# Kernel optimization log

Hardware: AMD Instinct MI355X
Metric: run time of the kernel (lower is better)

The kernel has to match this reference:

```python
import jax, jax.numpy as jnp
import numpy as np

STRIDE = 2  # ksize = [1, STRIDE, 1, 1]: unpool along height only
B, H, W, C = 8, 512, 256, 64


def setup_inputs() -> dict:
    key = jax.random.key(0)
    k1, k2 = jax.random.split(key)
    inputs = jax.random.normal(k1, (B, H, W, C), dtype=jnp.float32)
    # TF argmax-style flat indices into the per-batch output grid [2H, W, C]
    mask = jax.random.randint(k2, (B, H, W, C), 0, STRIDE * H * W * C, dtype=jnp.int64)
    return {"inputs": inputs, "mask": mask}


def reference(inputs, mask):
    b_, h, w, c = inputs.shape
    out_h = h * STRIDE  # output_shape = (B, stride*H, W, C)
    # Decode flat per-batch indices exactly as the TF layer does
    y = mask // (w * c)
    x = (mask % (w * c)) // c
    b = jnp.arange(b_, dtype=jnp.int64)[:, None, None, None]  # batch_range
    f = jnp.arange(c, dtype=jnp.int64)                        # feature_range
    # tf.scatter_nd sums duplicate indices; .at[].add matches that semantics
    out = jnp.zeros((b_, out_h, w, c), dtype=inputs.dtype)
    out = out.at[b, y, x, f].add(inputs)
    return out
```

## Files before the change

### kernel.cpp

```cpp
#include <hip/hip_runtime.h>


typedef unsigned int u32;
typedef unsigned short u16;
typedef unsigned long long u64;

typedef int   iv4 __attribute__((ext_vector_type(4)));
typedef float fv4 __attribute__((ext_vector_type(4)));

constexpr long long N_IN = 1LL << 26;
constexpr int SBS   = 8192;
constexpr int NSB   = (int)(N_IN / SBS);
constexpr int NBKT  = 1024;
constexpr int NWIN  = 8192;
constexpr int RSH   = 14;
constexpr int RSLOTS = 1 << RSH;
constexpr int SB_PER_B = 1024;

constexpr size_t OFF_RECA = 0;
constexpr size_t OFF_DIR  = (size_t)N_IN * 8;
constexpr size_t OFF_DIRT = OFF_DIR + (size_t)NSB * NBKT * 2;
constexpr size_t WS_FUSED = OFF_DIRT + (size_t)NWIN * SB_PER_B * 2;

__global__ __launch_bounds__(512) void passA(const float* __restrict__ in,
                                             const int* __restrict__ mask,
                                             u64* __restrict__ recA,
                                             u16* __restrict__ dir)
{
    __shared__ u32 cur[NBKT];
    __shared__ u32 wsum[8];
    __shared__ u64 sRec[SBS];
    const int tid = threadIdx.x;
    const int sb  = blockIdx.x;
    const int e0  = sb * SBS + tid * 16;

    const iv4* m4 = (const iv4*)mask + (e0 >> 2);
    const fv4* v4 = (const fv4*)in + (e0 >> 2);
    iv4 m0 = __builtin_nontemporal_load(m4 + 0);
    iv4 m1 = __builtin_nontemporal_load(m4 + 1);
    iv4 m2 = __builtin_nontemporal_load(m4 + 2);
    iv4 m3 = __builtin_nontemporal_load(m4 + 3);
    fv4 va = __builtin_nontemporal_load(v4 + 0);
    fv4 vb = __builtin_nontemporal_load(v4 + 1);
    fv4 vc = __builtin_nontemporal_load(v4 + 2);
    fv4 vd = __builtin_nontemporal_load(v4 + 3);
    const u32 bbits = ((u32)(e0 >> 23)) << 24;
    const u32 c0 = (u32)(e0 & 63);

    u32 tg[16]; float vv[16];
    tg[ 0] = bbits + (((u32)m0.x) & ~63u) + c0 +  0; vv[ 0] = va.x;
    tg[ 1] = bbits + (((u32)m0.y) & ~63u) + c0 +  1; vv[ 1] = va.y;
    tg[ 2] = bbits + (((u32)m0.z) & ~63u) + c0 +  2; vv[ 2] = va.z;
    tg[ 3] = bbits + (((u32)m0.w) & ~63u) + c0 +  3; vv[ 3] = va.w;
    tg[ 4] = bbits + (((u32)m1.x) & ~63u) + c0 +  4; vv[ 4] = vb.x;
    tg[ 5] = bbits + (((u32)m1.y) & ~63u) + c0 +  5; vv[ 5] = vb.y;
    tg[ 6] = bbits + (((u32)m1.z) & ~63u) + c0 +  6; vv[ 6] = vb.z;
    tg[ 7] = bbits + (((u32)m1.w) & ~63u) + c0 +  7; vv[ 7] = vb.w;
    tg[ 8] = bbits + (((u32)m2.x) & ~63u) + c0 +  8; vv[ 8] = vc.x;
    tg[ 9] = bbits + (((u32)m2.y) & ~63u) + c0 +  9; vv[ 9] = vc.y;
    tg[10] = bbits + (((u32)m2.z) & ~63u) + c0 + 10; vv[10] = vc.z;
    tg[11] = bbits + (((u32)m2.w) & ~63u) + c0 + 11; vv[11] = vc.w;
    tg[12] = bbits + (((u32)m3.x) & ~63u) + c0 + 12; vv[12] = vd.x;
    tg[13] = bbits + (((u32)m3.y) & ~63u) + c0 + 13; vv[13] = vd.y;
    tg[14] = bbits + (((u32)m3.z) & ~63u) + c0 + 14; vv[14] = vd.z;
    tg[15] = bbits + (((u32)m3.w) & ~63u) + c0 + 15; vv[15] = vd.w;

    cur[2 * tid] = 0;
    cur[2 * tid + 1] = 0;
    __syncthreads();
#pragma unroll
    for (int j = 0; j < 16; ++j) atomicAdd(&cur[(tg[j] >> RSH) & (NBKT - 1)], 1u);
    __syncthreads();

    {
        const int lane = tid & 63;
        const int wid  = tid >> 6;
        u32 a = cur[2 * tid];
        u32 b = cur[2 * tid + 1];
        u32 sum = a + b;
        u32 s = sum;
#pragma unroll
        for (int d = 1; d < 64; d <<= 1) {
            u32 n = __shfl_up(s, (unsigned)d, 64);
            if (lane >= d) s += n;
        }
        if (lane == 63) wsum[wid] = s;
        u32 exw = s - sum;
        __syncthreads();
        if (tid == 0) {
            u32 run = 0;
#pragma unroll
            for (int w = 0; w < 8; ++w) { u32 t2 = wsum[w]; wsum[w] = run; run += t2; }
        }
        __syncthreads();
        u32 start = wsum[wid] + exw;
        dir[(size_t)sb * NBKT + 2 * tid]     = (u16)start;
        dir[(size_t)sb * NBKT + 2 * tid + 1] = (u16)(start + a);
        cur[2 * tid]     = start;
        cur[2 * tid + 1] = start + a;
    }
    __syncthreads();

#pragma unroll
    for (int j = 0; j < 16; ++j) {
        u32 p = atomicAdd(&cur[(tg[j] >> RSH) & (NBKT - 1)], 1u);
        sRec[p] = ((u64)(tg[j] & (RSLOTS - 1)) << 32) | (u64)__float_as_uint(vv[j]);
    }
    __syncthreads();
#pragma unroll
    for (int k = 0; k < 16; ++k) {
        int i = tid + k * 512;
        recA[(size_t)sb * SBS + i] = sRec[i];
    }
}

__global__ __launch_bounds__(256) void tposeD(const u16* __restrict__ dir,
                                              u16* __restrict__ dirT)
{
    __shared__ u16 t[64][65];
    const int tx = threadIdx.x;
    const int ty = threadIdx.y;
    const int bb = blockIdx.z;
    const int sb0 = blockIdx.x * 64;
    const int lb0 = blockIdx.y * 64;
#pragma unroll
    for (int k = 0; k < 16; ++k) {
        int row = k * 4 + ty;
        t[row][tx] = dir[((size_t)(bb * SB_PER_B + sb0 + row)) * NBKT + lb0 + tx];
    }
    __syncthreads();
#pragma unroll
    for (int k = 0; k < 16; ++k) {
        int row = k * 4 + ty;
        dirT[((size_t)(bb * NBKT + lb0 + row)) * SB_PER_B + sb0 + tx] = t[tx][row];
    }
}

__global__ __launch_bounds__(1024, 8) void passC(const u64* __restrict__ recA,
                                                 const u16* __restrict__ dirT,
                                                 float* __restrict__ out)
{
    __shared__ float acc[RSLOTS];
    __shared__ u32 cSrc[SB_PER_B];
    __shared__ u16 cLen[SB_PER_B];
    const int tid = threadIdx.x;
    const int bid = blockIdx.x;
    const int w   = ((bid & 7) << 10) | (bid >> 3);
    const int bb  = w >> 10;
    const int lb  = w & (NBKT - 1);

    {
        u32 st = dirT[(size_t)w * SB_PER_B + tid];
        u32 en = (lb == NBKT - 1) ? (u32)SBS : (u32)dirT[(size_t)(w + 1) * SB_PER_B + tid];
        cSrc[tid] = (u32)(bb * SB_PER_B + tid) * (u32)SBS + st;
        cLen[tid] = (u16)(en - st);
    }
    {
        fv4 z = {0.f, 0.f, 0.f, 0.f};
        fv4* av = (fv4*)acc;
#pragma unroll
        for (int i = tid; i < RSLOTS / 4; i += 1024) av[i] = z;
    }
    __syncthreads();

    const int g  = tid >> 4;
    const int gl = tid & 15;
#pragma unroll
    for (int r = 0; r < 2; ++r) {
        u32 src[8]; int len[8]; u64 rec[8];
#pragma unroll
        for (int j = 0; j < 8; ++j) {
            int s = g + (r * 8 + j) * 64;
            src[j] = cSrc[s];
            len[j] = (int)cLen[s];
        }
#pragma unroll
        for (int j = 0; j < 8; ++j) rec[j] = recA[src[j] + gl];
#pragma unroll
        for (int j = 0; j < 8; ++j) {
            if (gl < len[j])
                atomicAdd(&acc[(u32)(rec[j] >> 32)], __uint_as_float((u32)rec[j]));
        }
#pragma unroll
        for (int j = 0; j < 8; ++j) {
            for (int off = gl + 16; off < len[j]; off += 16) {
                u64 rc = recA[src[j] + off];
                atomicAdd(&acc[(u32)(rc >> 32)], __uint_as_float((u32)rc));
            }
        }
    }
    __syncthreads();

    fv4* o4 = (fv4*)out + ((size_t)w << (RSH - 2));
    const fv4* a4 = (const fv4*)acc;
#pragma unroll
    for (int i = tid; i < RSLOTS / 4; i += 1024)
        __builtin_nontemporal_store(a4[i], o4 + i);
}

__global__ __launch_bounds__(256) void unmaxpool_scatter(
    const float* __restrict__ in, const int* __restrict__ mask,
    float* __restrict__ out)
{
    const long long n4 = N_IN / 4;
    long long gidx = (long long)blockIdx.x * blockDim.x + threadIdx.x;
    const long long stride = (long long)gridDim.x * blockDim.x;
    for (; gidx < n4; gidx += stride) {
        float4 v = reinterpret_cast<const float4*>(in)[gidx];
        int4 m = reinterpret_cast<const int4*>(mask)[gidx];
        long long i0 = gidx * 4;
        u32 ob = ((u32)(i0 >> 23)) << 24;
        u32 c0 = (u32)(i0 & 63);
        atomicAdd(&out[ob + (u32)(m.x & ~63) + c0 + 0], v.x);
        atomicAdd(&out[ob + (u32)(m.y & ~63) + c0 + 1], v.y);
        atomicAdd(&out[ob + (u32)(m.z & ~63) + c0 + 2], v.z);
        atomicAdd(&out[ob + (u32)(m.w & ~63) + c0 + 3], v.w);
    }
}

extern "C" void kernel_launch(void* const* d_in, const int* in_sizes, int n_in,
                              void* d_out, int out_size, void* d_ws, size_t ws_size,
                              hipStream_t stream) {
    const float* in = (const float*)d_in[0];
    const int* mask = (const int*)d_in[1];
    float* out = (float*)d_out;
    char* ws = (char*)d_ws;

    if (d_ws != nullptr && ws_size >= WS_FUSED) {
        u64* recA = (u64*)(ws + OFF_RECA);
        u16* dir  = (u16*)(ws + OFF_DIR);
        u16* dirT = (u16*)(ws + OFF_DIRT);
        passA<<<NSB, 512, 0, stream>>>(in, mask, recA, dir);
        tposeD<<<dim3(16, 16, 8), dim3(64, 4), 0, stream>>>(dir, dirT);
        passC<<<NWIN, 1024, 0, stream>>>(recA, dirT, out);
    } else {
        (void)hipMemsetAsync(out, 0, (size_t)out_size * sizeof(float), stream);
        unmaxpool_scatter<<<2048, 256, 0, stream>>>(in, mask, out);
    }
}
```

Before: 632.5 us.

## Load-balance passC record gathering via prefix-sum over segment lengths

Replaces the fixed 16-lanes-per-segment gather in passC with an exclusive prefix sum over per-superblock segment lengths. Each thread writes the source indices for its segment into a shared index buffer in 1024-entry rounds, and the whole block then processes one record per thread. This is meant to remove lane divergence and idle lanes from uneven segment lengths (about 8 records on average). In exchange it adds a block-wide scan, a serial per-thread fill loop, and two barriers per round, which may cost more than the imbalance it removes.

```diff
diff --git a/kernel.cpp b/kernel.cpp
--- a/kernel.cpp
+++ b/kernel.cpp
@@ -141,20 +141,31 @@
                                                  float* __restrict__ out)
 {
     __shared__ float acc[RSLOTS];
-    __shared__ u32 cSrc[SB_PER_B];
-    __shared__ u16 cLen[SB_PER_B];
+    __shared__ u32 cPre[SB_PER_B + 1];
+    __shared__ u32 srcIdx[1024];
+    __shared__ u32 wsum[16];
     const int tid = threadIdx.x;
     const int bid = blockIdx.x;
     const int w   = ((bid & 7) << 10) | (bid >> 3);
     const int bb  = w >> 10;
     const int lb  = w & (NBKT - 1);
 
-    {
-        u32 st = dirT[(size_t)w * SB_PER_B + tid];
-        u32 en = (lb == NBKT - 1) ? (u32)SBS : (u32)dirT[(size_t)(w + 1) * SB_PER_B + tid];
-        cSrc[tid] = (u32)(bb * SB_PER_B + tid) * (u32)SBS + st;
-        cLen[tid] = (u16)(en - st);
-    }
+    const u32 st = dirT[(size_t)w * SB_PER_B + tid];
+    const u32 en = (lb == NBKT - 1) ? (u32)SBS : (u32)dirT[(size_t)(w + 1) * SB_PER_B + tid];
+    const u32 len = en - st;
+    const u32 src = (u32)(bb * SB_PER_B + tid) * (u32)SBS + st;
+
+    const int lane = tid & 63;
+    const int wid  = tid >> 6;
+    u32 s = len;
+#pragma unroll
+    for (int d = 1; d < 64; d <<= 1) {
+        u32 n = __shfl_up(s, (unsigned)d, 64);
+        if (lane >= d) s += n;
+    }
+    if (lane == 63) wsum[wid] = s;
+    const u32 exw = s - len;
+
     {
         fv4 z = {0.f, 0.f, 0.f, 0.f};
         fv4* av = (fv4*)acc;
@@ -162,34 +173,34 @@
         for (int i = tid; i < RSLOTS / 4; i += 1024) av[i] = z;
     }
     __syncthreads();
-
-    const int g  = tid >> 4;
-    const int gl = tid & 15;
-#pragma unroll
-    for (int r = 0; r < 2; ++r) {
-        u32 src[8]; int len[8]; u64 rec[8];
-#pragma unroll
-        for (int j = 0; j < 8; ++j) {
-            int s = g + (r * 8 + j) * 64;
-            src[j] = cSrc[s];
-            len[j] = (int)cLen[s];
+    if (tid == 0) {
+        u32 run = 0;
+#pragma unroll
+        for (int ww = 0; ww < 16; ++ww) { u32 t2 = wsum[ww]; wsum[ww] = run; run += t2; }
+    }
+    __syncthreads();
+    const u32 pre = wsum[wid] + exw;
+    cPre[tid] = pre;
+    if (tid == SB_PER_B - 1) cPre[SB_PER_B] = pre + len;
+    __syncthreads();
+    const u32 total = cPre[SB_PER_B];
+    const int nsub = (int)((total + 1023u) >> 10);
+
+    for (int r = 0; r < nsub; ++r) {
+        const u32 r0 = (u32)r << 10;
+        const u32 r1 = r0 + 1024u;
+        u32 lo = pre > r0 ? pre : r0;
+        u32 hi = (pre + len < r1) ? (pre + len) : r1;
+        for (u32 q = lo; q < hi; ++q) srcIdx[q - r0] = src + (q - pre);
+        __syncthreads();
+        u32 n = total - r0; if (n > 1024u) n = 1024u;
+        if ((u32)tid < n) {
+            u32 si = srcIdx[tid];
+            u64 rec = recA[si];
+            atomicAdd(&acc[(u32)(rec >> 32)], __uint_as_float((u32)rec));
         }
-#pragma unroll
-        for (int j = 0; j < 8; ++j) rec[j] = recA[src[j] + gl];
-#pragma unroll
-        for (int j = 0; j < 8; ++j) {
-            if (gl < len[j])
-                atomicAdd(&acc[(u32)(rec[j] >> 32)], __uint_as_float((u32)rec[j]));
-        }
-#pragma unroll
-        for (int j = 0; j < 8; ++j) {
-            for (int off = gl + 16; off < len[j]; off += 16) {
-                u64 rc = recA[src[j] + off];
-                atomicAdd(&acc[(u32)(rc >> 32)], __uint_as_float((u32)rc));
-            }
-        }
-    }
-    __syncthreads();
+        __syncthreads();
+    }
 
     fv4* o4 = (fv4*)out + ((size_t)w << (RSH - 2));
     const fv4* a4 = (const fv4*)acc;
```

After: 742.4 us. 17.4% more time.

## Double superblock size in binning pass and restructure segment gather loop

Applied to the files above, without the earlier changes.

Doubles the superblock size handled by each passA block from 8192 to 16384 elements with 1024 threads, so there are half as many superblocks per batch. Each window in passC therefore gathers from 512 longer segments instead of 1024 short ones, and the gather loop is rewritten to handle up to 32 records per segment with simple conditionals. The intent is to cut per-segment overhead and wasted lanes on short segments in passC and to shrink the directory and transpose. In exchange, passA needs twice the shared memory per block (128KB of records), which lowers its occupancy, and passC loses the batched independent loads it had before.

```diff
diff --git a/kernel.cpp b/kernel.cpp
--- a/kernel.cpp
+++ b/kernel.cpp
@@ -9,26 +9,26 @@
 typedef float fv4 __attribute__((ext_vector_type(4)));
 
 constexpr long long N_IN = 1LL << 26;
-constexpr int SBS   = 8192;
+constexpr int SBS   = 16384;
 constexpr int NSB   = (int)(N_IN / SBS);
 constexpr int NBKT  = 1024;
 constexpr int NWIN  = 8192;
 constexpr int RSH   = 14;
 constexpr int RSLOTS = 1 << RSH;
-constexpr int SB_PER_B = 1024;
+constexpr int SB_PER_B = 512;
 
 constexpr size_t OFF_RECA = 0;
 constexpr size_t OFF_DIR  = (size_t)N_IN * 8;
 constexpr size_t OFF_DIRT = OFF_DIR + (size_t)NSB * NBKT * 2;
 constexpr size_t WS_FUSED = OFF_DIRT + (size_t)NWIN * SB_PER_B * 2;
 
-__global__ __launch_bounds__(512) void passA(const float* __restrict__ in,
-                                             const int* __restrict__ mask,
-                                             u64* __restrict__ recA,
-                                             u16* __restrict__ dir)
+__global__ __launch_bounds__(1024) void passA(const float* __restrict__ in,
+                                              const int* __restrict__ mask,
+                                              u64* __restrict__ recA,
+                                              u16* __restrict__ dir)
 {
     __shared__ u32 cur[NBKT];
-    __shared__ u32 wsum[8];
+    __shared__ u32 wsum[16];
     __shared__ u64 sRec[SBS];
     const int tid = threadIdx.x;
     const int sb  = blockIdx.x;
@@ -65,8 +65,7 @@
     tg[14] = bbits + (((u32)m3.z) & ~63u) + c0 + 14; vv[14] = vd.z;
     tg[15] = bbits + (((u32)m3.w) & ~63u) + c0 + 15; vv[15] = vd.w;
 
-    cur[2 * tid] = 0;
-    cur[2 * tid + 1] = 0;
+    cur[tid] = 0;
     __syncthreads();
 #pragma unroll
     for (int j = 0; j < 16; ++j) atomicAdd(&cur[(tg[j] >> RSH) & (NBKT - 1)], 1u);
@@ -75,29 +74,25 @@
     {
         const int lane = tid & 63;
         const int wid  = tid >> 6;
-        u32 a = cur[2 * tid];
-        u32 b = cur[2 * tid + 1];
-        u32 sum = a + b;
-        u32 s = sum;
+        u32 x = cur[tid];
+        u32 s = x;
 #pragma unroll
         for (int d = 1; d < 64; d <<= 1) {
             u32 n = __shfl_up(s, (unsigned)d, 64);
             if (lane >= d) s += n;
         }
         if (lane == 63) wsum[wid] = s;
-        u32 exw = s - sum;
+        u32 exw = s - x;
         __syncthreads();
         if (tid == 0) {
             u32 run = 0;
 #pragma unroll
-            for (int w = 0; w < 8; ++w) { u32 t2 = wsum[w]; wsum[w] = run; run += t2; }
+            for (int w = 0; w < 16; ++w) { u32 t2 = wsum[w]; wsum[w] = run; run += t2; }
         }
         __syncthreads();
         u32 start = wsum[wid] + exw;
-        dir[(size_t)sb * NBKT + 2 * tid]     = (u16)start;
-        dir[(size_t)sb * NBKT + 2 * tid + 1] = (u16)(start + a);
-        cur[2 * tid]     = start;
-        cur[2 * tid + 1] = start + a;
+        dir[(size_t)sb * NBKT + tid] = (u16)start;
+        cur[tid] = start;
     }
     __syncthreads();
 
@@ -109,7 +104,7 @@
     __syncthreads();
 #pragma unroll
     for (int k = 0; k < 16; ++k) {
-        int i = tid + k * 512;
+        int i = tid + k * 1024;
         recA[(size_t)sb * SBS + i] = sRec[i];
     }
 }
@@ -149,7 +144,7 @@
     const int bb  = w >> 10;
     const int lb  = w & (NBKT - 1);
 
-    {
+    if (tid < SB_PER_B) {
         u32 st = dirT[(size_t)w * SB_PER_B + tid];
         u32 en = (lb == NBKT - 1) ? (u32)SBS : (u32)dirT[(size_t)(w + 1) * SB_PER_B + tid];
         cSrc[tid] = (u32)(bb * SB_PER_B + tid) * (u32)SBS + st;
@@ -166,25 +161,19 @@
     const int g  = tid >> 4;
     const int gl = tid & 15;
 #pragma unroll
-    for (int r = 0; r < 2; ++r) {
-        u32 src[8]; int len[8]; u64 rec[8];
-#pragma unroll
-        for (int j = 0; j < 8; ++j) {
-            int s = g + (r * 8 + j) * 64;
-            src[j] = cSrc[s];
-            len[j] = (int)cLen[s];
-        }
-#pragma unroll
-        for (int j = 0; j < 8; ++j) rec[j] = recA[src[j] + gl];
-#pragma unroll
-        for (int j = 0; j < 8; ++j) {
-            if (gl < len[j])
-                atomicAdd(&acc[(u32)(rec[j] >> 32)], __uint_as_float((u32)rec[j]));
-        }
-#pragma unroll
-        for (int j = 0; j < 8; ++j) {
-            for (int off = gl + 16; off < len[j]; off += 16) {
-                u64 rc = recA[src[j] + off];
+    for (int j = 0; j < 8; ++j) {
+        const int s = g + j * 64;
+        const u32 src = cSrc[s];
+        const int len = (int)cLen[s];
+        u64 r0 = recA[src + gl];
+        if (gl < len)
+            atomicAdd(&acc[(u32)(r0 >> 32)], __uint_as_float((u32)r0));
+        if (len > 16) {
+            u64 r1 = recA[src + gl + 16];
+            if (gl + 16 < len)
+                atomicAdd(&acc[(u32)(r1 >> 32)], __uint_as_float((u32)r1));
+            for (int off = gl + 32; off < len; off += 16) {
+                u64 rc = recA[src + off];
                 atomicAdd(&acc[(u32)(rc >> 32)], __uint_as_float((u32)rc));
             }
         }
@@ -230,8 +219,8 @@
         u64* recA = (u64*)(ws + OFF_RECA);
         u16* dir  = (u16*)(ws + OFF_DIR);
         u16* dirT = (u16*)(ws + OFF_DIRT);
-        passA<<<NSB, 512, 0, stream>>>(in, mask, recA, dir);
-        tposeD<<<dim3(16, 16, 8), dim3(64, 4), 0, stream>>>(dir, dirT);
+        passA<<<NSB, 1024, 0, stream>>>(in, mask, recA, dir);
+        tposeD<<<dim3(8, 16, 8), dim3(64, 4), 0, stream>>>(dir, dirT);
         passC<<<NWIN, 1024, 0, stream>>>(recA, dirT, out);
     } else {
         (void)hipMemsetAsync(out, 0, (size_t)out_size * sizeof(float), stream);
```

Result: slower. 676.7 us (+7.0%).

## Double-buffer record fetch in passC via async global-to-LDS loads

Applied to the files above, without the earlier changes.

passC now stages the first 16 records of each source segment into a double-buffered LDS staging area using global_load_lds, so each batch's load is issued while the previous batch is accumulated. Each of the 8 batches covers 128 segments, and the segment tails beyond 16 records are handled serially by one thread per segment afterwards. The occupancy hint in launch_bounds is dropped and 32KB of extra shared memory is used. This may lower occupancy, and the serial tail loop could be slow when segments are long.

```diff
diff --git a/kernel.cpp b/kernel.cpp
--- a/kernel.cpp
+++ b/kernel.cpp
@@ -136,11 +136,12 @@
     }
 }
 
-__global__ __launch_bounds__(1024, 8) void passC(const u64* __restrict__ recA,
-                                                 const u16* __restrict__ dirT,
-                                                 float* __restrict__ out)
+__global__ __launch_bounds__(1024) void passC(const u64* __restrict__ recA,
+                                              const u16* __restrict__ dirT,
+                                              float* __restrict__ out)
 {
     __shared__ float acc[RSLOTS];
+    __shared__ u64 stage[2][2048];
     __shared__ u32 cSrc[SB_PER_B];
     __shared__ u16 cLen[SB_PER_B];
     const int tid = threadIdx.x;
@@ -155,6 +156,18 @@
         cSrc[tid] = (u32)(bb * SB_PER_B + tid) * (u32)SBS + st;
         cLen[tid] = (u16)(en - st);
     }
+    __syncthreads();
+
+    auto issue = [&](int b, int buf) {
+        const int c = (b << 7) + (tid >> 3);
+        const u64* gp = recA + (size_t)cSrc[c] + (size_t)((tid & 7) << 1);
+        void* lp = (void*)&stage[buf][(size_t)((tid >> 6) << 7)];
+        __builtin_amdgcn_global_load_lds(
+            (const __attribute__((address_space(1))) void*)gp,
+            (__attribute__((address_space(3))) void*)lp, 16, 0, 0);
+    };
+
+    issue(0, 0);
     {
         fv4 z = {0.f, 0.f, 0.f, 0.f};
         fv4* av = (fv4*)acc;
@@ -163,30 +176,30 @@
     }
     __syncthreads();
 
-    const int g  = tid >> 4;
-    const int gl = tid & 15;
-#pragma unroll
-    for (int r = 0; r < 2; ++r) {
-        u32 src[8]; int len[8]; u64 rec[8];
-#pragma unroll
-        for (int j = 0; j < 8; ++j) {
-            int s = g + (r * 8 + j) * 64;
-            src[j] = cSrc[s];
-            len[j] = (int)cLen[s];
-        }
-#pragma unroll
-        for (int j = 0; j < 8; ++j) rec[j] = recA[src[j] + gl];
-#pragma unroll
-        for (int j = 0; j < 8; ++j) {
-            if (gl < len[j])
-                atomicAdd(&acc[(u32)(rec[j] >> 32)], __uint_as_float((u32)rec[j]));
-        }
-#pragma unroll
-        for (int j = 0; j < 8; ++j) {
-            for (int off = gl + 16; off < len[j]; off += 16) {
-                u64 rc = recA[src[j] + off];
-                atomicAdd(&acc[(u32)(rc >> 32)], __uint_as_float((u32)rc));
-            }
+    int buf = 0;
+#pragma unroll 1
+    for (int b = 0; b < 8; ++b) {
+        if (b < 7) issue(b + 1, buf ^ 1);
+        {
+            const int c   = (b << 7) + (tid >> 3);
+            const int len = (int)cLen[c];
+            const int r0  = (tid & 7) << 1;
+            u64 a0 = stage[buf][2 * tid];
+            u64 a1 = stage[buf][2 * tid + 1];
+            if (r0 < len)
+                atomicAdd(&acc[(u32)(a0 >> 32)], __uint_as_float((u32)a0));
+            if (r0 + 1 < len)
+                atomicAdd(&acc[(u32)(a1 >> 32)], __uint_as_float((u32)a1));
+        }
+        __syncthreads();
+        buf ^= 1;
+    }
+
+    {
+        const int len = (int)cLen[tid];
+        for (int off = 16; off < len; ++off) {
+            u64 rc = recA[(size_t)cSrc[tid] + off];
+            atomicAdd(&acc[(u32)(rc >> 32)], __uint_as_float((u32)rc));
         }
     }
     __syncthreads();
```

New measurement: 855.5 us. 1.35x slower.
